# Kernel optimization log

Measured on AMD Instinct MI355X. Metric: run time of the kernel, lower is better.

## Reference

```python
import jax, jax.numpy as jnp
import numpy as np


def setup_inputs() -> dict:
    key = jax.random.key(0)
    k1, k2 = jax.random.split(key)
    B, N, M, D = 16, 2048, 2048, 128
    Q = jax.random.normal(k1, (B, N, D), dtype=jnp.float32)
    KV = jax.random.normal(k2, (B, D, M), dtype=jnp.float32)
    log_sigmas = jnp.zeros((1,), dtype=jnp.float32)
    return {"Q": Q, "KV": KV, "log_sigmas": log_sigmas}


def reference(Q, KV, log_sigmas):
    # Q: [B, N, D], KV: [B, D, M]
    # ||q||^2 per row, ||k||^2 per column (norm squared == sum of squares)
    Q_sq = jnp.sum(Q * Q, axis=-1, keepdims=True)        # [B, N, 1]
    KV_sq = jnp.sum(KV * KV, axis=-2, keepdims=True)     # [B, 1, M]
    QKV = jnp.einsum('bnd,bdm->bnm', Q, KV)              # [B, N, M]
    inv_two_sigma_sq = -0.5 / jnp.exp(2.0 * log_sigmas)  # scalar (shape [1])
    # exp(-||q-k||^2 / (2 sigma^2)) fused epilogue
    out = jnp.exp(inv_two_sigma_sq * (Q_sq + KV_sq - 2.0 * QKV))
    return out
```

## Files before the change

### kernel.cpp

```cpp
#include <hip/hip_runtime.h>


#define B_  16
#define N_  2048
#define M_  2048
#define D_  128

typedef _Float16 half8 __attribute__((ext_vector_type(8)));
typedef float    f32x4 __attribute__((ext_vector_type(4)));

__global__ __launch_bounds__(256) void prep_q(const float* __restrict__ Q,
                                              _Float16* __restrict__ Qh,
                                              float* __restrict__ Qsq) {
    const int row  = blockIdx.x * 4 + (threadIdx.x >> 6);
    const int lane = threadIdx.x & 63;
    const float2 v = reinterpret_cast<const float2*>(Q + (size_t)row * D_)[lane];
    float sq = v.x * v.x + v.y * v.y;
    union { _Float16 h[2]; unsigned int u; } pk;
    pk.h[0] = (_Float16)v.x;
    pk.h[1] = (_Float16)v.y;
    reinterpret_cast<unsigned int*>(Qh + (size_t)row * D_)[lane] = pk.u;
    #pragma unroll
    for (int off = 32; off > 0; off >>= 1) sq += __shfl_down(sq, off, 64);
    if (lane == 0) Qsq[row] = sq;
}

__global__ __launch_bounds__(256) void prep_kv(const float* __restrict__ KV,
                                               _Float16* __restrict__ KTh,
                                               float* __restrict__ Ksq) {
    const int b = blockIdx.y;
    const int m = blockIdx.x * 256 + threadIdx.x;
    const float* src = KV + (size_t)b * D_ * M_ + m;
    _Float16*   dst = KTh + ((size_t)b * M_ + m) * D_;
    float sq = 0.f;
    #pragma unroll 2
    for (int k0 = 0; k0 < D_; k0 += 8) {
        union { _Float16 h[8]; int4 v; } buf;
        #pragma unroll
        for (int j = 0; j < 8; ++j) {
            const float v = src[(size_t)(k0 + j) * M_];
            sq += v * v;
            buf.h[j] = (_Float16)v;
        }
        *reinterpret_cast<int4*>(dst + k0) = buf.v;
    }
    Ksq[(size_t)b * M_ + m] = sq;
}

__global__ __launch_bounds__(256, 2) void gauss_gemm(
    const _Float16* __restrict__ Qh, const _Float16* __restrict__ KTh,
    const float* __restrict__ Qsq,  const float* __restrict__ Ksq,
    const float* __restrict__ ls,   float* __restrict__ out) {
    __shared__ __align__(16) char smem[132 * 128 * 4];
    _Float16* Ash = (_Float16*)smem;
    _Float16* Bsh = (_Float16*)(smem + 32768);

    const int b    = blockIdx.y;
    const int bx   = blockIdx.x;
    const int n0   = (bx >> 4) << 7;
    const int m0   = (bx & 15) << 7;
    const int tid  = threadIdx.x;
    const int wave = tid >> 6;
    const int lane = tid & 63;

    const _Float16* Ag = Qh  + ((size_t)b * N_ + n0) * D_;
    const _Float16* Bg = KTh + ((size_t)b * M_ + m0) * D_;

    #pragma unroll
    for (int i = 0; i < 8; ++i) {
        const int chunk = wave * 8 + i;
        const int r     = chunk * 4 + (lane >> 4);
        const int g     = (lane & 15) ^ (r & 7);
        const int goff  = r * 128 + g * 8;
        __builtin_amdgcn_global_load_lds(
            (const __attribute__((address_space(1))) unsigned int*)(Ag + goff),
            (__attribute__((address_space(3))) unsigned int*)(&Ash[chunk * 512]), 16, 0, 0);
        __builtin_amdgcn_global_load_lds(
            (const __attribute__((address_space(1))) unsigned int*)(Bg + goff),
            (__attribute__((address_space(3))) unsigned int*)(&Bsh[chunk * 512]), 16, 0, 0);
    }
    __syncthreads();

    const int wr = (wave >> 1) * 64;
    const int wc = (wave & 1) * 64;
    const int lm = lane & 15;
    const int kq = lane >> 4;
    const int sw = lm & 7;

    f32x4 acc[4][4] = {};
    #pragma unroll
    for (int ks = 0; ks < 128; ks += 32) {
        const int gl = (ks >> 3) + kq;
        half8 af[4], bf[4];
        #pragma unroll
        for (int r = 0; r < 4; ++r)
            af[r] = *reinterpret_cast<const half8*>(
                &Ash[(wr + r * 16 + lm) * 128 + ((gl ^ sw) << 3)]);
        #pragma unroll
        for (int c = 0; c < 4; ++c)
            bf[c] = *reinterpret_cast<const half8*>(
                &Bsh[(wc + c * 16 + lm) * 128 + ((gl ^ sw) << 3)]);
        #pragma unroll
        for (int r = 0; r < 4; ++r)
            #pragma unroll
            for (int c = 0; c < 4; ++c)
                acc[r][c] = __builtin_amdgcn_mfma_f32_16x16x32_f16(af[r], bf[c], acc[r][c], 0, 0, 0);
    }

    const float inv2s = -0.5f * __expf(-2.0f * ls[0]);
    const float cm2   = -2.0f * inv2s;
    const int l4 = (lane >> 4) * 4;
    const float* qsq = Qsq + (size_t)b * N_ + n0;
    const float* ksq = Ksq + (size_t)b * M_ + m0;

    float ksv[4];
    #pragma unroll
    for (int c = 0; c < 4; ++c) ksv[c] = ksq[wc + c * 16 + lm];
    float qsv[4][4];
    #pragma unroll
    for (int r = 0; r < 4; ++r)
        #pragma unroll
        for (int i = 0; i < 4; ++i) qsv[r][i] = qsq[wr + r * 16 + l4 + i];

    __syncthreads();
    float* Csh = (float*)smem;

    #pragma unroll
    for (int r = 0; r < 4; ++r) {
        #pragma unroll
        for (int i = 0; i < 4; ++i) {
            const int row = wr + r * 16 + l4 + i;
            #pragma unroll
            for (int c = 0; c < 4; ++c) {
                const float t = fmaf(cm2, acc[r][c][i], inv2s * (qsv[r][i] + ksv[c]));
                Csh[row * 132 + wc + c * 16 + lm] = __expf(t);
            }
        }
    }
    __syncthreads();

    float* Cb = out + ((size_t)b * N_ + n0) * (size_t)M_ + m0;
    const int trow = tid >> 5;
    const int tcol = (tid & 31) << 2;
    #pragma unroll
    for (int it = 0; it < 16; ++it) {
        const int row = it * 8 + trow;
        const f32x4 v = *reinterpret_cast<const f32x4*>(&Csh[row * 132 + tcol]);
        *reinterpret_cast<f32x4*>(&Cb[(size_t)row * M_ + tcol]) = v;
    }
}

extern "C" void kernel_launch(void* const* d_in, const int* in_sizes, int n_in,
                              void* d_out, int out_size, void* d_ws, size_t ws_size,
                              hipStream_t stream) {
    const float* Q  = (const float*)d_in[0];
    const float* KV = (const float*)d_in[1];
    const float* ls = (const float*)d_in[2];
    float* out = (float*)d_out;

    char* ws = (char*)d_ws;
    _Float16* Qh  = (_Float16*)ws;
    _Float16* KTh = (_Float16*)(ws + (size_t)8 * 1024 * 1024);
    float*    Qsq = (float*)(ws + (size_t)16 * 1024 * 1024);
    float*    Ksq = (float*)(ws + (size_t)16 * 1024 * 1024 + 128 * 1024);

    prep_q <<<dim3(B_ * N_ / 4), 256, 0, stream>>>(Q, Qh, Qsq);
    prep_kv<<<dim3(M_ / 256, B_), 256, 0, stream>>>(KV, KTh, Ksq);
    gauss_gemm<<<dim3(256, B_), 256, 0, stream>>>(Qh, KTh, Qsq, Ksq, ls, out);
}
```

Measured before the change: 319.6 us.

## Fuse fp16 conversion and norm computation into single GEMM kernel

```diff
diff --git a/kernel.cpp b/kernel.cpp
--- a/kernel.cpp
+++ b/kernel.cpp
@@ -9,144 +9,135 @@
 typedef _Float16 half8 __attribute__((ext_vector_type(8)));
 typedef float    f32x4 __attribute__((ext_vector_type(4)));
 
-__global__ __launch_bounds__(256) void prep_q(const float* __restrict__ Q,
-                                              _Float16* __restrict__ Qh,
-                                              float* __restrict__ Qsq) {
-    const int row  = blockIdx.x * 4 + (threadIdx.x >> 6);
-    const int lane = threadIdx.x & 63;
-    const float2 v = reinterpret_cast<const float2*>(Q + (size_t)row * D_)[lane];
-    float sq = v.x * v.x + v.y * v.y;
-    union { _Float16 h[2]; unsigned int u; } pk;
-    pk.h[0] = (_Float16)v.x;
-    pk.h[1] = (_Float16)v.y;
-    reinterpret_cast<unsigned int*>(Qh + (size_t)row * D_)[lane] = pk.u;
-    #pragma unroll
-    for (int off = 32; off > 0; off >>= 1) sq += __shfl_down(sq, off, 64);
-    if (lane == 0) Qsq[row] = sq;
-}
+__global__ __launch_bounds__(256, 3) void gauss_fused(
+    const float* __restrict__ Q, const float* __restrict__ KV,
+    const float* __restrict__ ls, float* __restrict__ out) {
 
-__global__ __launch_bounds__(256) void prep_kv(const float* __restrict__ KV,
-                                               _Float16* __restrict__ KTh,
-                                               float* __restrict__ Ksq) {
-    const int b = blockIdx.y;
-    const int m = blockIdx.x * 256 + threadIdx.x;
-    const float* src = KV + (size_t)b * D_ * M_ + m;
-    _Float16*   dst = KTh + ((size_t)b * M_ + m) * D_;
-    float sq = 0.f;
-    #pragma unroll 2
-    for (int k0 = 0; k0 < D_; k0 += 8) {
-        union { _Float16 h[8]; int4 v; } buf;
-        #pragma unroll
-        for (int j = 0; j < 8; ++j) {
-            const float v = src[(size_t)(k0 + j) * M_];
-            sq += v * v;
-            buf.h[j] = (_Float16)v;
-        }
-        *reinterpret_cast<int4*>(dst + k0) = buf.v;
-    }
-    Ksq[(size_t)b * M_ + m] = sq;
-}
+    __shared__ __align__(16) _Float16 Ash[128 * 64];
+    __shared__ __align__(16) _Float16 Bsh[128 * 64];
+    __shared__ float Qs[128];
+    __shared__ float Ks[128];
 
-__global__ __launch_bounds__(256, 2) void gauss_gemm(
-    const _Float16* __restrict__ Qh, const _Float16* __restrict__ KTh,
-    const float* __restrict__ Qsq,  const float* __restrict__ Ksq,
-    const float* __restrict__ ls,   float* __restrict__ out) {
-    __shared__ __align__(16) char smem[132 * 128 * 4];
-    _Float16* Ash = (_Float16*)smem;
-    _Float16* Bsh = (_Float16*)(smem + 32768);
+    const int b  = blockIdx.y;
+    int bx = blockIdx.x;
+    bx = ((bx & 7) << 5) | (bx >> 3);
+    const int n0 = (bx >> 4) << 7;
+    const int m0 = (bx & 15) << 7;
 
-    const int b    = blockIdx.y;
-    const int bx   = blockIdx.x;
-    const int n0   = (bx >> 4) << 7;
-    const int m0   = (bx & 15) << 7;
     const int tid  = threadIdx.x;
     const int wave = tid >> 6;
     const int lane = tid & 63;
 
-    const _Float16* Ag = Qh  + ((size_t)b * N_ + n0) * D_;
-    const _Float16* Bg = KTh + ((size_t)b * M_ + m0) * D_;
+    const int r     = tid >> 1;
+    const int kc    = (tid & 1) << 5;
+    const int gbase = (tid & 1) << 2;
+    const int sw    = r & 7;
+
+    const float* Ag = Q  + ((size_t)b * N_ + n0 + r) * D_ + kc;
+    const float* Bg = KV + (size_t)b * D_ * M_ + (size_t)kc * M_ + m0 + r;
+
+    const int wr  = (wave >> 1) << 6;
+    const int wc  = (wave & 1) << 6;
+    const int lm  = lane & 15;
+    const int kq  = lane >> 4;
+    const int fsw = lm & 7;
+
+    float sqA = 0.f, sqB = 0.f;
+    f32x4 acc[4][4] = {};
 
     #pragma unroll
-    for (int i = 0; i < 8; ++i) {
-        const int chunk = wave * 8 + i;
-        const int r     = chunk * 4 + (lane >> 4);
-        const int g     = (lane & 15) ^ (r & 7);
-        const int goff  = r * 128 + g * 8;
-        __builtin_amdgcn_global_load_lds(
-            (const __attribute__((address_space(1))) unsigned int*)(Ag + goff),
-            (__attribute__((address_space(3))) unsigned int*)(&Ash[chunk * 512]), 16, 0, 0);
-        __builtin_amdgcn_global_load_lds(
-            (const __attribute__((address_space(1))) unsigned int*)(Bg + goff),
-            (__attribute__((address_space(3))) unsigned int*)(&Bsh[chunk * 512]), 16, 0, 0);
-    }
-    __syncthreads();
+    for (int h = 0; h < 2; ++h) {
+        f32x4 av[8];
+        #pragma unroll
+        for (int j = 0; j < 8; ++j)
+            av[j] = *reinterpret_cast<const f32x4*>(Ag + h * 64 + j * 4);
+        float bv[32];
+        #pragma unroll
+        for (int j = 0; j < 32; ++j)
+            bv[j] = Bg[(size_t)(h * 64 + j) * M_];
 
-    const int wr = (wave >> 1) * 64;
-    const int wc = (wave & 1) * 64;
-    const int lm = lane & 15;
-    const int kq = lane >> 4;
-    const int sw = lm & 7;
+        if (h) __syncthreads();
 
-    f32x4 acc[4][4] = {};
-    #pragma unroll
-    for (int ks = 0; ks < 128; ks += 32) {
-        const int gl = (ks >> 3) + kq;
-        half8 af[4], bf[4];
         #pragma unroll
-        for (int r = 0; r < 4; ++r)
-            af[r] = *reinterpret_cast<const half8*>(
-                &Ash[(wr + r * 16 + lm) * 128 + ((gl ^ sw) << 3)]);
+        for (int g = 0; g < 4; ++g) {
+            union { _Float16 hh[8]; half8 v; } pa;
+            #pragma unroll
+            for (int p = 0; p < 2; ++p) {
+                const f32x4 v = av[g * 2 + p];
+                sqA = fmaf(v.x, v.x, sqA);
+                sqA = fmaf(v.y, v.y, sqA);
+                sqA = fmaf(v.z, v.z, sqA);
+                sqA = fmaf(v.w, v.w, sqA);
+                pa.hh[p * 4 + 0] = (_Float16)v.x;
+                pa.hh[p * 4 + 1] = (_Float16)v.y;
+                pa.hh[p * 4 + 2] = (_Float16)v.z;
+                pa.hh[p * 4 + 3] = (_Float16)v.w;
+            }
+            *reinterpret_cast<half8*>(&Ash[r * 64 + (((gbase + g) ^ sw) << 3)]) = pa.v;
+
+            union { _Float16 hh[8]; half8 v; } pb;
+            #pragma unroll
+            for (int e = 0; e < 8; ++e) {
+                const float x = bv[g * 8 + e];
+                sqB = fmaf(x, x, sqB);
+                pb.hh[e] = (_Float16)x;
+            }
+            *reinterpret_cast<half8*>(&Bsh[r * 64 + (((gbase + g) ^ sw) << 3)]) = pb.v;
+        }
+
+        if (h) {
+            sqA += __shfl_xor(sqA, 1, 64);
+            sqB += __shfl_xor(sqB, 1, 64);
+            if ((tid & 1) == 0) { Qs[r] = sqA; Ks[r] = sqB; }
+        }
+        __syncthreads();
+
         #pragma unroll
-        for (int c = 0; c < 4; ++c)
-            bf[c] = *reinterpret_cast<const half8*>(
-                &Bsh[(wc + c * 16 + lm) * 128 + ((gl ^ sw) << 3)]);
-        #pragma unroll
-        for (int r = 0; r < 4; ++r)
+        for (int s = 0; s < 2; ++s) {
+            const int gl = (s << 2) + kq;
+            half8 af[4], bf[4];
             #pragma unroll
-            for (int c = 0; c < 4; ++c)
-                acc[r][c] = __builtin_amdgcn_mfma_f32_16x16x32_f16(af[r], bf[c], acc[r][c], 0, 0, 0);
+            for (int rr = 0; rr < 4; ++rr)
+                af[rr] = *reinterpret_cast<const half8*>(
+                    &Ash[(wr + rr * 16 + lm) * 64 + ((gl ^ fsw) << 3)]);
+            #pragma unroll
+            for (int cc = 0; cc < 4; ++cc)
+                bf[cc] = *reinterpret_cast<const half8*>(
+                    &Bsh[(wc + cc * 16 + lm) * 64 + ((gl ^ fsw) << 3)]);
+            #pragma unroll
+            for (int rr = 0; rr < 4; ++rr)
+                #pragma unroll
+                for (int cc = 0; cc < 4; ++cc)
+                    acc[rr][cc] = __builtin_amdgcn_mfma_f32_16x16x32_f16(
+                        af[rr], bf[cc], acc[rr][cc], 0, 0, 0);
+        }
     }
 
     const float inv2s = -0.5f * __expf(-2.0f * ls[0]);
     const float cm2   = -2.0f * inv2s;
-    const int l4 = (lane >> 4) * 4;
-    const float* qsq = Qsq + (size_t)b * N_ + n0;
-    const float* ksq = Ksq + (size_t)b * M_ + m0;
+    const int   l4    = kq << 2;
 
     float ksv[4];
     #pragma unroll
-    for (int c = 0; c < 4; ++c) ksv[c] = ksq[wc + c * 16 + lm];
+    for (int cc = 0; cc < 4; ++cc) ksv[cc] = inv2s * Ks[wc + cc * 16 + lm];
     float qsv[4][4];
     #pragma unroll
-    for (int r = 0; r < 4; ++r)
+    for (int rr = 0; rr < 4; ++rr)
         #pragma unroll
-        for (int i = 0; i < 4; ++i) qsv[r][i] = qsq[wr + r * 16 + l4 + i];
+        for (int i = 0; i < 4; ++i) qsv[rr][i] = inv2s * Qs[wr + rr * 16 + l4 + i];
 
-    __syncthreads();
-    float* Csh = (float*)smem;
-
+    float* Cb = out + ((size_t)b * N_ + n0 + wr + l4) * M_ + m0 + wc + lm;
     #pragma unroll
-    for (int r = 0; r < 4; ++r) {
+    for (int rr = 0; rr < 4; ++rr) {
         #pragma unroll
         for (int i = 0; i < 4; ++i) {
-            const int row = wr + r * 16 + l4 + i;
+            float* p = Cb + (size_t)(rr * 16 + i) * M_;
             #pragma unroll
-            for (int c = 0; c < 4; ++c) {
-                const float t = fmaf(cm2, acc[r][c][i], inv2s * (qsv[r][i] + ksv[c]));
-                Csh[row * 132 + wc + c * 16 + lm] = __expf(t);
+            for (int cc = 0; cc < 4; ++cc) {
+                const float t = fmaf(cm2, acc[rr][cc][i], qsv[rr][i] + ksv[cc]);
+                p[cc * 16] = __expf(t);
             }
         }
-    }
-    __syncthreads();
-
-    float* Cb = out + ((size_t)b * N_ + n0) * (size_t)M_ + m0;
-    const int trow = tid >> 5;
-    const int tcol = (tid & 31) << 2;
-    #pragma unroll
-    for (int it = 0; it < 16; ++it) {
-        const int row = it * 8 + trow;
-        const f32x4 v = *reinterpret_cast<const f32x4*>(&Csh[row * 132 + tcol]);
-        *reinterpret_cast<f32x4*>(&Cb[(size_t)row * M_ + tcol]) = v;
     }
 }
 
@@ -158,13 +149,5 @@
     const float* ls = (const float*)d_in[2];
     float* out = (float*)d_out;
 
-    char* ws = (char*)d_ws;
-    _Float16* Qh  = (_Float16*)ws;
-    _Float16* KTh = (_Float16*)(ws + (size_t)8 * 1024 * 1024);
-    float*    Qsq = (float*)(ws + (size_t)16 * 1024 * 1024);
-    float*    Ksq = (float*)(ws + (size_t)16 * 1024 * 1024 + 128 * 1024);
-
-    prep_q <<<dim3(B_ * N_ / 4), 256, 0, stream>>>(Q, Qh, Qsq);
-    prep_kv<<<dim3(M_ / 256, B_), 256, 0, stream>>>(KV, KTh, Ksq);
-    gauss_gemm<<<dim3(256, B_), 256, 0, stream>>>(Qh, KTh, Qsq, Ksq, ls, out);
+    gauss_fused<<<dim3(256, B_), 256, 0, stream>>>(Q, KV, ls, out);
 }
```

After: 358.3 us. +12.1%, slower.

## Split K into two staged halves, shrink LDS, and store epilogue directly

Applied to the files above, without the earlier changes.

```diff
diff --git a/kernel.cpp b/kernel.cpp
--- a/kernel.cpp
+++ b/kernel.cpp
@@ -47,13 +47,12 @@
     Ksq[(size_t)b * M_ + m] = sq;
 }
 
-__global__ __launch_bounds__(256, 2) void gauss_gemm(
+__global__ __launch_bounds__(256, 3) void gauss_gemm(
     const _Float16* __restrict__ Qh, const _Float16* __restrict__ KTh,
     const float* __restrict__ Qsq,  const float* __restrict__ Ksq,
     const float* __restrict__ ls,   float* __restrict__ out) {
-    __shared__ __align__(16) char smem[132 * 128 * 4];
-    _Float16* Ash = (_Float16*)smem;
-    _Float16* Bsh = (_Float16*)(smem + 32768);
+    __shared__ __align__(16) _Float16 Ash[128 * 64];
+    __shared__ __align__(16) _Float16 Bsh[128 * 64];
 
     const int b    = blockIdx.y;
     const int bx   = blockIdx.x;
@@ -66,87 +65,103 @@
     const _Float16* Ag = Qh  + ((size_t)b * N_ + n0) * D_;
     const _Float16* Bg = KTh + ((size_t)b * M_ + m0) * D_;
 
+    int goff[4];
     #pragma unroll
-    for (int i = 0; i < 8; ++i) {
-        const int chunk = wave * 8 + i;
-        const int r     = chunk * 4 + (lane >> 4);
-        const int g     = (lane & 15) ^ (r & 7);
-        const int goff  = r * 128 + g * 8;
-        __builtin_amdgcn_global_load_lds(
-            (const __attribute__((address_space(1))) unsigned int*)(Ag + goff),
-            (__attribute__((address_space(3))) unsigned int*)(&Ash[chunk * 512]), 16, 0, 0);
-        __builtin_amdgcn_global_load_lds(
-            (const __attribute__((address_space(1))) unsigned int*)(Bg + goff),
-            (__attribute__((address_space(3))) unsigned int*)(&Bsh[chunk * 512]), 16, 0, 0);
+    for (int j = 0; j < 4; ++j) {
+        const int gi = j * 256 + tid;
+        const int r  = gi >> 3;
+        const int gc = gi & 7;
+        goff[j] = r * D_ + ((gc ^ (r & 7)) << 3);
     }
+    const int dbase = wave * 512;
+
+    auto STAGE = [&](int h) {
+        #pragma unroll
+        for (int j = 0; j < 4; ++j) {
+            __builtin_amdgcn_global_load_lds(
+                (const __attribute__((address_space(1))) unsigned int*)(Ag + h * 64 + goff[j]),
+                (__attribute__((address_space(3))) unsigned int*)(&Ash[j * 2048 + dbase]), 16, 0, 0);
+            __builtin_amdgcn_global_load_lds(
+                (const __attribute__((address_space(1))) unsigned int*)(Bg + h * 64 + goff[j]),
+                (__attribute__((address_space(3))) unsigned int*)(&Bsh[j * 2048 + dbase]), 16, 0, 0);
+        }
+    };
+
+    const int wr  = (wave >> 1) << 6;
+    const int wc  = (wave & 1) << 6;
+    const int lm  = lane & 15;
+    const int kq  = lane >> 4;
+    const int fsw = lm & 7;
+
+    auto READ = [&](half8 af[2][4], half8 bf[2][4]) {
+        #pragma unroll
+        for (int s = 0; s < 2; ++s) {
+            const int pc = ((((s << 2) + kq) ^ fsw) << 3);
+            #pragma unroll
+            for (int rr = 0; rr < 4; ++rr)
+                af[s][rr] = *reinterpret_cast<const half8*>(
+                    &Ash[(wr + rr * 16 + lm) * 64 + pc]);
+            #pragma unroll
+            for (int cc = 0; cc < 4; ++cc)
+                bf[s][cc] = *reinterpret_cast<const half8*>(
+                    &Bsh[(wc + cc * 16 + lm) * 64 + pc]);
+        }
+    };
+
+    f32x4 acc[4][4] = {};
+    auto MFMA = [&](half8 af[2][4], half8 bf[2][4]) {
+        #pragma unroll
+        for (int s = 0; s < 2; ++s)
+            #pragma unroll
+            for (int rr = 0; rr < 4; ++rr)
+                #pragma unroll
+                for (int cc = 0; cc < 4; ++cc)
+                    acc[rr][cc] = __builtin_amdgcn_mfma_f32_16x16x32_f16(
+                        af[s][rr], bf[s][cc], acc[rr][cc], 0, 0, 0);
+    };
+
+    STAGE(0);
     __syncthreads();
 
-    const int wr = (wave >> 1) * 64;
-    const int wc = (wave & 1) * 64;
-    const int lm = lane & 15;
-    const int kq = lane >> 4;
-    const int sw = lm & 7;
+    half8 a0[2][4], b0[2][4];
+    READ(a0, b0);
+    __syncthreads();
 
-    f32x4 acc[4][4] = {};
-    #pragma unroll
-    for (int ks = 0; ks < 128; ks += 32) {
-        const int gl = (ks >> 3) + kq;
-        half8 af[4], bf[4];
-        #pragma unroll
-        for (int r = 0; r < 4; ++r)
-            af[r] = *reinterpret_cast<const half8*>(
-                &Ash[(wr + r * 16 + lm) * 128 + ((gl ^ sw) << 3)]);
-        #pragma unroll
-        for (int c = 0; c < 4; ++c)
-            bf[c] = *reinterpret_cast<const half8*>(
-                &Bsh[(wc + c * 16 + lm) * 128 + ((gl ^ sw) << 3)]);
-        #pragma unroll
-        for (int r = 0; r < 4; ++r)
-            #pragma unroll
-            for (int c = 0; c < 4; ++c)
-                acc[r][c] = __builtin_amdgcn_mfma_f32_16x16x32_f16(af[r], bf[c], acc[r][c], 0, 0, 0);
-    }
+    STAGE(1);
+    MFMA(a0, b0);
+    __syncthreads();
+
+    half8 a1[2][4], b1[2][4];
+    READ(a1, b1);
+    MFMA(a1, b1);
 
     const float inv2s = -0.5f * __expf(-2.0f * ls[0]);
     const float cm2   = -2.0f * inv2s;
-    const int l4 = (lane >> 4) * 4;
+    const int   l4    = kq << 2;
     const float* qsq = Qsq + (size_t)b * N_ + n0;
     const float* ksq = Ksq + (size_t)b * M_ + m0;
 
     float ksv[4];
     #pragma unroll
-    for (int c = 0; c < 4; ++c) ksv[c] = ksq[wc + c * 16 + lm];
+    for (int cc = 0; cc < 4; ++cc) ksv[cc] = inv2s * ksq[wc + cc * 16 + lm];
     float qsv[4][4];
     #pragma unroll
-    for (int r = 0; r < 4; ++r)
+    for (int rr = 0; rr < 4; ++rr)
         #pragma unroll
-        for (int i = 0; i < 4; ++i) qsv[r][i] = qsq[wr + r * 16 + l4 + i];
+        for (int i = 0; i < 4; ++i) qsv[rr][i] = inv2s * qsq[wr + rr * 16 + l4 + i];
 
-    __syncthreads();
-    float* Csh = (float*)smem;
-
+    float* Cb = out + ((size_t)b * N_ + n0 + wr + l4) * M_ + m0 + wc + lm;
     #pragma unroll
-    for (int r = 0; r < 4; ++r) {
+    for (int rr = 0; rr < 4; ++rr) {
         #pragma unroll
         for (int i = 0; i < 4; ++i) {
-            const int row = wr + r * 16 + l4 + i;
+            float* p = Cb + (size_t)(rr * 16 + i) * M_;
             #pragma unroll
-            for (int c = 0; c < 4; ++c) {
-                const float t = fmaf(cm2, acc[r][c][i], inv2s * (qsv[r][i] + ksv[c]));
-                Csh[row * 132 + wc + c * 16 + lm] = __expf(t);
+            for (int cc = 0; cc < 4; ++cc) {
+                const float t = fmaf(cm2, acc[rr][cc][i], qsv[rr][i] + ksv[cc]);
+                p[cc * 16] = __expf(t);
             }
         }
-    }
-    __syncthreads();
-
-    float* Cb = out + ((size_t)b * N_ + n0) * (size_t)M_ + m0;
-    const int trow = tid >> 5;
-    const int tcol = (tid & 31) << 2;
-    #pragma unroll
-    for (int it = 0; it < 16; ++it) {
-        const int row = it * 8 + trow;
-        const f32x4 v = *reinterpret_cast<const f32x4*>(&Csh[row * 132 + tcol]);
-        *reinterpret_cast<f32x4*>(&Cb[(size_t)row * M_ + tcol]) = v;
     }
 }
 
```

Measured after the change: 307.8 us. 1.04x faster.
